# Performance work log

Hardware: AMD Instinct MI355X
Metric: run time of the kernel (lower is better)

## Reference

```python
import jax, jax.numpy as jnp
import numpy as np

N = 10000      # nodes (attention_adj_matrix_shape = (N, N))
E = 320000     # edges, avg degree 32
D_IN = 256     # input feature dim
D_H = 256      # hidden_units = [256]
ALPHA = 0.2    # leaky_relu slope for attention activation


def setup_inputs() -> dict:
    key = jax.random.key(0)
    k_x, k_src, k_dst, k_w1, k_b1, k_wa, k_ba = jax.random.split(key, 7)
    node_features = jax.random.normal(k_x, (N, D_IN), dtype=jnp.float32)
    # edges sorted by source column (tf.math.segment_sum requires sorted segment ids)
    src = jnp.sort(jax.random.randint(k_src, (E,), 0, N))
    dst = jax.random.randint(k_dst, (E,), 0, N)
    edges = jnp.stack([src, dst], axis=1).astype(jnp.int64)
    # hidden_layer: single Dense(256) (linear, keras Dense default activation=None)
    W1 = jax.random.normal(k_w1, (D_IN, D_H), dtype=jnp.float32) / np.sqrt(D_IN)
    b1 = jnp.zeros((D_H,), dtype=jnp.float32)
    # attention_layer: Dense(1) then activation
    Wa = jax.random.normal(k_wa, (2 * D_H, 1), dtype=jnp.float32) / np.sqrt(2 * D_H)
    ba = jnp.zeros((1,), dtype=jnp.float32)
    return {"node_features": node_features, "edges": edges,
            "W1": W1, "b1": b1, "Wa": Wa, "ba": ba}


def reference(node_features, edges, W1, b1, Wa, ba):
    n = node_features.shape[0]
    # hidden projection
    feats = node_features @ W1 + b1                       # [N, D_H]
    src, dst = edges[:, 0], edges[:, 1]
    # pairwise gather + concat: [E, 2*D_H]
    pair = jnp.concatenate([feats[src], feats[dst]], axis=1)
    scores = jax.nn.leaky_relu((pair @ Wa + ba)[:, 0], ALPHA)  # [E]
    # segment softmax over source node (matches exp / segment_sum / gather)
    ex = jnp.exp(scores)
    denom = jax.ops.segment_sum(ex, src, num_segments=n)       # [N]
    alpha = ex / denom[src]                                     # [E]
    # dense scatter of attention weights (scatter_nd sums duplicates)
    A = jnp.zeros((n, n), dtype=feats.dtype).at[src, dst].add(alpha)
    # add_self_features=False -> plain aggregate
    return A @ feats                                            # [N, D_H]
```

## Files before the change

kernel.cpp:

```cpp
#include <hip/hip_runtime.h>
#include <hip/hip_bf16.h>

#define N_NODES 10000
#define E_EDGES 320000
#define D 256
#define LRELU_ALPHA 0.2f


using short8  = __attribute__((ext_vector_type(8))) short;
using floatx4 = __attribute__((ext_vector_type(4))) float;
using bf16 = __hip_bfloat16;

__device__ __forceinline__ float bu2f(unsigned short u) {
    return __uint_as_float((unsigned)u << 16);
}
__device__ __forceinline__ unsigned short f2bu(float f) {
    union { bf16 b; unsigned short u; } cv;
    cv.b = __float2bfloat16(f);
    return cv.u;
}

__global__ __launch_bounds__(256) void wprep(const float* __restrict__ W1,
                                             bf16* __restrict__ W1f) {
    const int id = blockIdx.x * 256 + threadIdx.x;
    const int j = id & 7, l = (id >> 3) & 63, t = (id >> 9) & 15, s = id >> 13;
    const int k = s * 32 + (l >> 4) * 8 + j;
    const int n = t * 16 + (l & 15);
    W1f[id] = __float2bfloat16(W1[k * D + n]);
}

__global__ __launch_bounds__(256) void gemm_mfma(const float* __restrict__ X,
                                                 const bf16* __restrict__ W1f,
                                                 const float* __restrict__ b1,
                                                 const float* __restrict__ Wa,
                                                 bf16* __restrict__ featsb,
                                                 float* __restrict__ a_src,
                                                 float* __restrict__ a_dst) {
    const int w = threadIdx.x >> 6, l = threadIdx.x & 63;
    const int quad = l >> 4, lan = l & 15;
    const int row0 = blockIdx.x * 16;

    floatx4 acc[4] = {{0.f, 0.f, 0.f, 0.f}, {0.f, 0.f, 0.f, 0.f},
                      {0.f, 0.f, 0.f, 0.f}, {0.f, 0.f, 0.f, 0.f}};

    const float4* Ax = (const float4*)(X + (size_t)(row0 + lan) * D);
    const short8* B8 = (const short8*)W1f;

    #pragma unroll
    for (int s = 0; s < 8; ++s) {
        const float4 u = Ax[s * 8 + quad * 2];
        const float4 v = Ax[s * 8 + quad * 2 + 1];
        short8 af;
        af[0] = (short)f2bu(u.x); af[1] = (short)f2bu(u.y);
        af[2] = (short)f2bu(u.z); af[3] = (short)f2bu(u.w);
        af[4] = (short)f2bu(v.x); af[5] = (short)f2bu(v.y);
        af[6] = (short)f2bu(v.z); af[7] = (short)f2bu(v.w);
        #pragma unroll
        for (int t = 0; t < 4; ++t) {
            const short8 bf = B8[(s * 16 + (4 * w + t)) * 64 + l];
            acc[t] = __builtin_amdgcn_mfma_f32_16x16x32_bf16(af, bf, acc[t], 0, 0, 0);
        }
    }

    float p1[4] = {0.f, 0.f, 0.f, 0.f}, p2[4] = {0.f, 0.f, 0.f, 0.f};
    #pragma unroll
    for (int t = 0; t < 4; ++t) {
        const int n = (4 * w + t) * 16 + lan;
        const float bias = b1[n], wa1 = Wa[n], wa2 = Wa[D + n];
        #pragma unroll
        for (int r = 0; r < 4; ++r) {
            const float v = acc[t][r] + bias;
            featsb[(size_t)(row0 + quad * 4 + r) * D + n] = __float2bfloat16(v);
            p1[r] += v * wa1;
            p2[r] += v * wa2;
        }
    }

    __shared__ float red1[4][16], red2[4][16];
    #pragma unroll
    for (int r = 0; r < 4; ++r) {
        #pragma unroll
        for (int off = 1; off < 16; off <<= 1) {
            p1[r] += __shfl_xor(p1[r], off);
            p2[r] += __shfl_xor(p2[r], off);
        }
        if (lan == 0) { red1[w][quad * 4 + r] = p1[r]; red2[w][quad * 4 + r] = p2[r]; }
    }
    __syncthreads();
    if (threadIdx.x < 16) {
        const int m = threadIdx.x;
        a_src[row0 + m] = red1[0][m] + red1[1][m] + red1[2][m] + red1[3][m];
        a_dst[row0 + m] = red2[0][m] + red2[1][m] + red2[2][m] + red2[3][m];
    }
}

__global__ __launch_bounds__(256) void prep(const int* __restrict__ raw,
                                            const float* __restrict__ a_src,
                                            const float* __restrict__ a_dst,
                                            const float* __restrict__ ba,
                                            int2* __restrict__ edata,
                                            int* __restrict__ row_start) {
    bool is64 = true;
    #pragma unroll
    for (int t = 0; t < 16; ++t)
        if (raw[2 * t + 1] != 0) is64 = false;

    int e = blockIdx.x * 256 + threadIdx.x;
    if (e >= E_EDGES) return;
    int s, d, sprev;
    if (is64) { s = raw[4 * e]; d = raw[4 * e + 2]; sprev = e ? raw[4 * e - 4] : -1; }
    else      { s = raw[2 * e]; d = raw[2 * e + 1]; sprev = e ? raw[2 * e - 2] : -1; }

    float sc = a_src[s] + a_dst[d] + ba[0];
    sc = (sc > 0.f) ? sc : LRELU_ALPHA * sc;
    edata[e] = make_int2(d << 9, __float_as_int(expf(sc)));

    for (int r = sprev + 1; r <= s; ++r) row_start[r] = e;
    if (e == E_EDGES - 1)
        for (int r = s + 1; r <= N_NODES; ++r) row_start[r] = E_EDGES;
}

__global__ __launch_bounds__(256) void aggregate(const int2* __restrict__ edata,
                                                 const int* __restrict__ row_start,
                                                 const unsigned short* __restrict__ featsb,
                                                 float* __restrict__ out) {
    __shared__ int2 els[4][64];
    const int wv = threadIdx.x >> 6, l = threadIdx.x & 63;
    const int i = blockIdx.x * 4 + wv;
    const int rs = row_start[i], re = row_start[i + 1];
    const char* Fb = (const char*)featsb;

    float4 acc = {0.f, 0.f, 0.f, 0.f};
    float dsum = 0.f;

    for (int e = rs; e < re; e += 64) {
        const int cnt = min(64, re - e);
        if (l < cnt) els[wv][l] = edata[e + l];
        __builtin_amdgcn_wave_barrier();

        int j = 0;
        for (; j + 8 <= cnt; j += 8) {
            #pragma unroll
            for (int u = 0; u < 8; ++u) {
                const int2 ed = els[wv][j + u];
                const ushort4 f = *(const ushort4*)(Fb + (size_t)(unsigned)ed.x + l * 8);
                const float x = __int_as_float(ed.y);
                acc.x += x * bu2f(f.x); acc.y += x * bu2f(f.y);
                acc.z += x * bu2f(f.z); acc.w += x * bu2f(f.w);
                dsum += x;
            }
        }
        for (; j < cnt; ++j) {
            const int2 ed = els[wv][j];
            const ushort4 f = *(const ushort4*)(Fb + (size_t)(unsigned)ed.x + l * 8);
            const float x = __int_as_float(ed.y);
            acc.x += x * bu2f(f.x); acc.y += x * bu2f(f.y);
            acc.z += x * bu2f(f.z); acc.w += x * bu2f(f.w);
            dsum += x;
        }
        __builtin_amdgcn_wave_barrier();
    }

    const float inv = (re > rs) ? 1.f / dsum : 0.f;
    float4 o;
    o.x = acc.x * inv; o.y = acc.y * inv; o.z = acc.z * inv; o.w = acc.w * inv;
    ((float4*)out)[(size_t)i * 64 + l] = o;
}

extern "C" void kernel_launch(void* const* d_in, const int* in_sizes, int n_in,
                              void* d_out, int out_size, void* d_ws, size_t ws_size,
                              hipStream_t stream) {
    const float* X     = (const float*)d_in[0];
    const int*   edges = (const int*)d_in[1];
    const float* W1    = (const float*)d_in[2];
    const float* b1    = (const float*)d_in[3];
    const float* Wa    = (const float*)d_in[4];
    const float* ba    = (const float*)d_in[5];
    float* out = (float*)d_out;

    bf16* featsb = (bf16*)d_ws;
    bf16* W1f    = featsb + (size_t)N_NODES * D;
    float* a_src = (float*)(W1f + 65536);
    float* a_dst = a_src + N_NODES;
    int2*  edata = (int2*)(a_dst + N_NODES);
    int*   row_start = (int*)(edata + E_EDGES);

    wprep<<<65536 / 256, 256, 0, stream>>>(W1, W1f);
    gemm_mfma<<<N_NODES / 16, 256, 0, stream>>>(X, W1f, b1, Wa, featsb, a_src, a_dst);
    prep<<<(E_EDGES + 255) / 256, 256, 0, stream>>>(edges, a_src, a_dst, ba, edata, row_start);
    aggregate<<<N_NODES / 4, 256, 0, stream>>>(edata, row_start,
                                               (const unsigned short*)featsb, out);
}
```

Before: 102.8 us.

## Split aggregation into two feature-half passes and vectorize edge loads in prep

The aggregation kernel is split into two launches, each covering 128 of the 256 feature columns. This halves the working set of the gathered bf16 feature table (about 2.5 MB per pass), so it is more likely to stay in L2 during the random gathers. The cost is reading the edge list and row offsets twice, with narrower 4-byte loads per lane. The prep kernel now loads each edge as a vector and takes the previous source id via a wave shuffle instead of a second global load. It also drops the bounds check, which relies on E being a multiple of 256.

```diff
diff --git a/kernel.cpp b/kernel.cpp
--- a/kernel.cpp
+++ b/kernel.cpp
@@ -105,11 +105,18 @@
     for (int t = 0; t < 16; ++t)
         if (raw[2 * t + 1] != 0) is64 = false;
 
-    int e = blockIdx.x * 256 + threadIdx.x;
-    if (e >= E_EDGES) return;
-    int s, d, sprev;
-    if (is64) { s = raw[4 * e]; d = raw[4 * e + 2]; sprev = e ? raw[4 * e - 4] : -1; }
-    else      { s = raw[2 * e]; d = raw[2 * e + 1]; sprev = e ? raw[2 * e - 2] : -1; }
+    const int e = blockIdx.x * 256 + threadIdx.x;
+    int s, d;
+    if (is64) {
+        const int4 v = ((const int4*)raw)[e];
+        s = v.x; d = v.z;
+    } else {
+        const int2 v = ((const int2*)raw)[e];
+        s = v.x; d = v.y;
+    }
+    int sprev = __shfl_up(s, 1);
+    if ((threadIdx.x & 63) == 0)
+        sprev = (e == 0) ? -1 : raw[is64 ? (4 * e - 4) : (2 * e - 2)];
 
     float sc = a_src[s] + a_dst[d] + ba[0];
     sc = (sc > 0.f) ? sc : LRELU_ALPHA * sc;
@@ -120,17 +127,18 @@
         for (int r = s + 1; r <= N_NODES; ++r) row_start[r] = E_EDGES;
 }
 
-__global__ __launch_bounds__(256) void aggregate(const int2* __restrict__ edata,
-                                                 const int* __restrict__ row_start,
-                                                 const unsigned short* __restrict__ featsb,
-                                                 float* __restrict__ out) {
+__global__ __launch_bounds__(256) void aggregate_half(const int2* __restrict__ edata,
+                                                      const int* __restrict__ row_start,
+                                                      const unsigned short* __restrict__ featsb,
+                                                      float* __restrict__ out,
+                                                      const int half) {
     __shared__ int2 els[4][64];
     const int wv = threadIdx.x >> 6, l = threadIdx.x & 63;
     const int i = blockIdx.x * 4 + wv;
     const int rs = row_start[i], re = row_start[i + 1];
-    const char* Fb = (const char*)featsb;
-
-    float4 acc = {0.f, 0.f, 0.f, 0.f};
+    const char* Fb = (const char*)featsb + half * 256 + l * 4;
+
+    float2 acc = {0.f, 0.f};
     float dsum = 0.f;
 
     for (int e = rs; e < re; e += 64) {
@@ -143,28 +151,29 @@
             #pragma unroll
             for (int u = 0; u < 8; ++u) {
                 const int2 ed = els[wv][j + u];
-                const ushort4 f = *(const ushort4*)(Fb + (size_t)(unsigned)ed.x + l * 8);
+                const unsigned int f = *(const unsigned int*)(Fb + (size_t)(unsigned)ed.x);
                 const float x = __int_as_float(ed.y);
-                acc.x += x * bu2f(f.x); acc.y += x * bu2f(f.y);
-                acc.z += x * bu2f(f.z); acc.w += x * bu2f(f.w);
+                acc.x += x * bu2f((unsigned short)(f & 0xffff));
+                acc.y += x * bu2f((unsigned short)(f >> 16));
                 dsum += x;
             }
         }
         for (; j < cnt; ++j) {
             const int2 ed = els[wv][j];
-            const ushort4 f = *(const ushort4*)(Fb + (size_t)(unsigned)ed.x + l * 8);
+            const unsigned int f = *(const unsigned int*)(Fb + (size_t)(unsigned)ed.x);
             const float x = __int_as_float(ed.y);
-            acc.x += x * bu2f(f.x); acc.y += x * bu2f(f.y);
-            acc.z += x * bu2f(f.z); acc.w += x * bu2f(f.w);
+            acc.x += x * bu2f((unsigned short)(f & 0xffff));
+            acc.y += x * bu2f((unsigned short)(f >> 16));
             dsum += x;
         }
         __builtin_amdgcn_wave_barrier();
     }
 
     const float inv = (re > rs) ? 1.f / dsum : 0.f;
-    float4 o;
-    o.x = acc.x * inv; o.y = acc.y * inv; o.z = acc.z * inv; o.w = acc.w * inv;
-    ((float4*)out)[(size_t)i * 64 + l] = o;
+    float2 o;
+    o.x = acc.x * inv;
+    o.y = acc.y * inv;
+    ((float2*)(out + (size_t)i * D + half * 128))[l] = o;
 }
 
 extern "C" void kernel_launch(void* const* d_in, const int* in_sizes, int n_in,
@@ -187,7 +196,9 @@
 
     wprep<<<65536 / 256, 256, 0, stream>>>(W1, W1f);
     gemm_mfma<<<N_NODES / 16, 256, 0, stream>>>(X, W1f, b1, Wa, featsb, a_src, a_dst);
-    prep<<<(E_EDGES + 255) / 256, 256, 0, stream>>>(edges, a_src, a_dst, ba, edata, row_start);
-    aggregate<<<N_NODES / 4, 256, 0, stream>>>(edata, row_start,
-                                               (const unsigned short*)featsb, out);
-}
+    prep<<<E_EDGES / 256, 256, 0, stream>>>(edges, a_src, a_dst, ba, edata, row_start);
+    aggregate_half<<<N_NODES / 4, 256, 0, stream>>>(edata, row_start,
+                                                    (const unsigned short*)featsb, out, 0);
+    aggregate_half<<<N_NODES / 4, 256, 0, stream>>>(edata, row_start,
+                                                    (const unsigned short*)featsb, out, 1);
+}
```

Measured after the change: 106.0 us. 3.1% more time.
